# Kernel tuning notes

Measured on AMD Instinct MI355X. Metric: run time of the kernel, lower is better.

## Reference

```python
import jax, jax.numpy as jnp
import numpy as np
import math

H_MAX = 0.05  # hardcoded in ode_solve


def setup_inputs() -> dict:
    key = jax.random.key(0)
    k0, k1, k2, k3 = jax.random.split(key, 4)
    bs, dim, u_dim, hidden, time_len = 4096, 256, 64, 1024, 11
    z0 = jax.random.normal(k0, (bs, dim), jnp.float32)
    u = jax.random.normal(k1, (bs, u_dim), jnp.float32)
    t = jnp.arange(time_len, dtype=jnp.float32) * 0.05  # uniform grid, dt = h_max
    W1 = jax.random.normal(k2, (dim + u_dim, hidden), jnp.float32) / np.float32(np.sqrt(dim + u_dim))
    b1 = jnp.zeros((hidden,), jnp.float32)
    W2 = jax.random.normal(k3, (hidden, dim), jnp.float32) / np.float32(np.sqrt(hidden))
    b2 = jnp.zeros((dim,), jnp.float32)
    return {"z0": z0, "u": u, "t": t, "W1": W1, "b1": b1, "W2": W2, "b2": b2}


def reference(z0, u, t, W1, b1, W2, b2):
    """NeuralODE.forward with return_whole_sequence=True.
    Euler-integrates dz/dt = f(z, u, t) between consecutive grid points of t.
    f is the ODEF: tanh([z, u] @ W1 + b1) @ W2 + b2 (autonomous, stimulus-driven).
    Returns z of shape [time_len, bs, dim].
    """
    t_np = np.asarray(t)  # step counts are static (trace-time) quantities

    def f(z):  # [bs, dim] -> [bs, dim]
        h = jnp.tanh(jnp.concatenate([z, u], axis=-1) @ W1 + b1)
        return h @ W2 + b2

    zs = [z0]
    z = z0
    for i_t in range(t_np.shape[0] - 1):
        t0f, t1f = float(t_np[i_t]), float(t_np[i_t + 1])
        n_steps = int(math.ceil(abs(t1f - t0f) / H_MAX))
        h = jnp.float32((t1f - t0f) / n_steps)

        def euler_step(zc, _):
            return zc + h * f(zc), None

        z, _ = jax.lax.scan(euler_step, z, None, length=n_steps)
        zs.append(z)
    return jnp.stack(zs, axis=0)  # [time_len, bs, dim]
```

## Files before the change

kernel.cpp:

```cpp
#include <hip/hip_runtime.h>
#include <hip/hip_bf16.h>

#define BS   4096
#define DIM  256
#define UD   64
#define HID  1024
#define KCAT 320
#define ROWS 16

typedef __attribute__((ext_vector_type(8))) short bf16x8;
typedef __attribute__((ext_vector_type(4))) float f32x4;


__global__ void NeuralODE_91036126806381_kernel() {}

__device__ __forceinline__ float rd_any(const void* p, long idx, int isbf) {
    if (isbf) return __bfloat162float(((const __hip_bfloat16*)p)[idx]);
    return ((const float*)p)[idx];
}

__device__ __forceinline__ int sniff_bf16(const void* p) {
    const unsigned* w = (const unsigned*)p;
    int pass = 0;
    for (int i = 0; i < 64; ++i) {
        unsigned h = w[i] & 0xFFFFu;
        unsigned e = (h >> 7) & 0xFFu;
        if (h == 0u || h == 0x8000u || (e >= 96u && e <= 140u)) ++pass;
    }
    return pass >= 48 ? 1 : 0;
}

__device__ __forceinline__ float tanh_dev(float x) {
    float ax = fminf(fabsf(x), 15.0f);
    float e = __expf(-2.0f * ax);
    float r = (1.0f - e) * __builtin_amdgcn_rcpf(1.0f + e);
    return (x < 0.0f) ? -r : r;
}

__device__ __forceinline__ bf16x8 ld8(const __hip_bfloat16* p) {
    return *(const bf16x8*)p;
}

__global__ void plan_kernel(const void* __restrict__ t_raw,
                            const void* __restrict__ z0r,
                            const void* __restrict__ candA,
                            const void* __restrict__ candB,
                            const void* __restrict__ W1r,
                            float* __restrict__ h_arr, int* __restrict__ flags)
{
    if (threadIdx.x != 0 || blockIdx.x != 0) return;

    flags[0] = sniff_bf16(z0r);
    flags[1] = sniff_bf16(candA);
    flags[2] = sniff_bf16(candB);
    flags[3] = sniff_bf16(W1r);

    float mA = 0.0f;
    for (int i = 0; i < 256; ++i) {
        float v = fabsf(rd_any(candA, i, flags[1]));
        if (v > mA) mA = v;
    }
    flags[6] = (mA < 0.25f) ? 1 : 0;

    const unsigned tw0 = ((const unsigned*)t_raw)[0];
    const int t_bf16 = (tw0 != 0u) ? 1 : 0;

    float tv[11];
    for (int i = 0; i < 11; ++i) tv[i] = rd_any(t_raw, i, t_bf16);

    for (int i = 0; i < 10; ++i) {
        double dt = (double)tv[i + 1] - (double)tv[i];
        double r  = __builtin_fabs(dt) / 0.05;
        int n = (int)__builtin_ceil(r);
        if (n < 1) n = 1;
        if (n > 2) n = 2;
        float h = (float)(dt / (double)n);
        h_arr[2 * i]     = h;
        h_arr[2 * i + 1] = (n >= 2) ? h : 0.0f;
    }
}

__global__ __launch_bounds__(256) void prep_kernel(
    const void* __restrict__ W1r,
    const void* __restrict__ candA, const void* __restrict__ candB,
    const void* __restrict__ z0r,
    const void* __restrict__ b1r,  const void* __restrict__ b2r,
    const int* __restrict__ flags,
    __hip_bfloat16* __restrict__ w1p, __hip_bfloat16* __restrict__ w2p,
    __hip_bfloat16* __restrict__ zcat,
    float* __restrict__ zf, float* __restrict__ b1f, float* __restrict__ b2f,
    float* __restrict__ out0)
{
    const int swap = flags[6];
    const void* ur   = swap ? candB : candA;
    const void* W2r  = swap ? candA : candB;
    const int uflag  = swap ? flags[2] : flags[1];
    const int w2flag = swap ? flags[1] : flags[2];

    int i = blockIdx.x * 256 + threadIdx.x;
    if (i < 327680) {
        int k = i >> 10, n = i & 1023;
        int C = n >> 4, fm = n & 15;
        int kt = k >> 5, q = (k >> 3) & 3, e = k & 7;
        w1p[((C * 40 + kt * 4 + q) * 16 + fm) * 8 + e] =
            __float2bfloat16(rd_any(W1r, i, flags[3]));
    } else if (i < 589824) {
        int j = i - 327680;
        int k = j >> 8, n = j & 255;
        int C = n >> 4, fm = n & 15;
        int kt = k >> 5, q = (k >> 3) & 3, e = k & 7;
        w2p[((C * 128 + kt * 4 + q) * 16 + fm) * 8 + e] =
            __float2bfloat16(rd_any(W2r, j, w2flag));
    } else if (i < 851968) {
        int j = i - 589824;
        int r = j >> 6, c = j & 63;
        zcat[(long)r * KCAT + DIM + c] = __float2bfloat16(rd_any(ur, j, uflag));
    } else if (i < 1900544) {
        int j = i - 851968;
        int r = j >> 8, c = j & 255;
        float v = rd_any(z0r, j, flags[0]);
        zf[j] = v;
        zcat[(long)r * KCAT + c] = __float2bfloat16(v);
        out0[j] = v;
    } else if (i < 1901568) {
        int j = i - 1900544;
        b1f[j] = rd_any(b1r, j, sniff_bf16(b1r));
    } else if (i < 1901824) {
        int j = i - 1901568;
        b2f[j] = rd_any(b2r, j, sniff_bf16(b2r));
    }
}

__global__ __launch_bounds__(1024) void ode_kernel(
    const __hip_bfloat16* __restrict__ w1p,
    const __hip_bfloat16* __restrict__ w2p,
    const float* __restrict__ b1f, const float* __restrict__ b2f,
    const __hip_bfloat16* __restrict__ zcat0,
    const float* __restrict__ zf0,
    float* __restrict__ out,
    const float* __restrict__ h_arr)
{
    __shared__ __align__(16) __hip_bfloat16 apack[10 * 4 * 16 * 8];
    __shared__ __align__(16) __hip_bfloat16 Hpack[32 * 4 * 16 * 8];

    const int b0   = blockIdx.x * ROWS;
    const int tid  = threadIdx.x;
    const int lane = tid & 63;
    const int wv   = tid >> 6;
    const int fm   = lane & 15;
    const int q    = lane >> 4;
    const int cl   = lane & 15;
    const int rq   = (lane >> 4) * 4;

    for (int idx = tid; idx < ROWS * KCAT; idx += 1024) {
        int row = idx / KCAT, c = idx - row * KCAT;
        apack[(((c >> 5) * 4 + ((c & 31) >> 3)) * 16 + row) * 8 + (c & 7)] =
            zcat0[(long)(b0 + row) * KCAT + c];
    }

    float zreg[4];
#pragma unroll
    for (int r = 0; r < 4; ++r)
        zreg[r] = zf0[(long)(b0 + rq + r) * DIM + wv * 16 + cl];

    float b1r[4];
#pragma unroll
    for (int j = 0; j < 4; ++j) b1r[j] = b1f[(wv * 4 + j) * 16 + cl];
    const float b2r = b2f[wv * 16 + cl];

    __syncthreads();

    for (int iv = 0; iv < 10; ++iv) {
#pragma unroll 1
        for (int s = 0; s < 2; ++s) {
            const float h = h_arr[iv * 2 + s];
            if (h != 0.0f) {
                bf16x8 a[10];
#pragma unroll
                for (int kt = 0; kt < 10; ++kt)
                    a[kt] = *(const bf16x8*)&apack[((kt * 4 + q) * 16 + fm) * 8];

#pragma unroll
                for (int j = 0; j < 4; ++j) {
                    const int C = wv * 4 + j;
                    const __hip_bfloat16* wp =
                        w1p + ((long)(C * 40 + q) * 16 + fm) * 8;
                    f32x4 acc0 = (f32x4){0.f, 0.f, 0.f, 0.f};
                    f32x4 acc1 = (f32x4){0.f, 0.f, 0.f, 0.f};
#pragma unroll
                    for (int kt = 0; kt < 10; kt += 2) {
                        acc0 = __builtin_amdgcn_mfma_f32_16x16x32_bf16(
                            a[kt], ld8(wp + (long)kt * 512), acc0, 0, 0, 0);
                        acc1 = __builtin_amdgcn_mfma_f32_16x16x32_bf16(
                            a[kt + 1], ld8(wp + (long)(kt + 1) * 512), acc1, 0, 0, 0);
                    }
                    const int colb = C * 16 + cl;
                    const int hbase =
                        ((colb >> 5) * 4 + ((colb & 31) >> 3)) * 128 + (colb & 7);
#pragma unroll
                    for (int r = 0; r < 4; ++r) {
                        float v = acc0[r] + acc1[r] + b1r[j];
                        Hpack[hbase + (rq + r) * 8] = __float2bfloat16(tanh_dev(v));
                    }
                }
                __syncthreads();

                f32x4 zacc0 = (f32x4){0.f, 0.f, 0.f, 0.f};
                f32x4 zacc1 = (f32x4){0.f, 0.f, 0.f, 0.f};
                const __hip_bfloat16* wq =
                    w2p + ((long)(wv * 128 + q) * 16 + fm) * 8;
#pragma unroll 8
                for (int kt = 0; kt < 32; kt += 2) {
                    bf16x8 aH0 = *(const bf16x8*)&Hpack[((kt * 4 + q) * 16 + fm) * 8];
                    bf16x8 aH1 = *(const bf16x8*)&Hpack[(((kt + 1) * 4 + q) * 16 + fm) * 8];
                    zacc0 = __builtin_amdgcn_mfma_f32_16x16x32_bf16(
                        aH0, ld8(wq + (long)kt * 512), zacc0, 0, 0, 0);
                    zacc1 = __builtin_amdgcn_mfma_f32_16x16x32_bf16(
                        aH1, ld8(wq + (long)(kt + 1) * 512), zacc1, 0, 0, 0);
                }

                const int col = wv * 16 + cl;
                const int abase =
                    ((col >> 5) * 4 + ((col & 31) >> 3)) * 128 + (col & 7);
#pragma unroll
                for (int r = 0; r < 4; ++r) {
                    float v = zreg[r] + h * (zacc0[r] + zacc1[r] + b2r);
                    zreg[r] = v;
                    apack[abase + (rq + r) * 8] = __float2bfloat16(v);
                }
                __syncthreads();
            }
        }
        float* os = out + (long)(iv + 1) * BS * DIM;
#pragma unroll
        for (int r = 0; r < 4; ++r)
            os[(long)(b0 + rq + r) * DIM + wv * 16 + cl] = zreg[r];
    }
}

extern "C" void kernel_launch(void* const* d_in, const int* in_sizes, int n_in,
                              void* d_out, int out_size, void* d_ws, size_t ws_size,
                              hipStream_t stream) {
    const void *z0 = 0, *t = 0, *W1 = 0, *b1 = 0, *b2 = 0;
    const void *candA = 0, *candB = 0;
    for (int i = 0; i < n_in; ++i) {
        int s = in_sizes[i];
        if      (s == 1048576) z0 = d_in[i];
        else if (s == 327680)  W1 = d_in[i];
        else if (s == 262144)  { if (!candA) candA = d_in[i]; else candB = d_in[i]; }
        else if (s == 1024)    b1 = d_in[i];
        else if (s == 256)     b2 = d_in[i];
        else if (s == 11)      t  = d_in[i];
    }
    if (!z0 || !W1 || !candA || !candB || !b1 || !b2 || !t) {
        z0 = d_in[0]; candA = d_in[1]; t = d_in[2];
        W1 = d_in[3]; b1 = d_in[4]; candB = d_in[5]; b2 = d_in[6];
    }

    float* out = (float*)d_out;

    char* ws = (char*)d_ws;
    int*            flags = (int*)  (ws + 0);
    float*          h_arr = (float*)(ws + 64);
    float*          b1f   = (float*)(ws + 4096);
    float*          b2f   = (float*)(ws + 8192);
    __hip_bfloat16* w1p   = (__hip_bfloat16*)(ws + 16384);
    __hip_bfloat16* w2p   = (__hip_bfloat16*)(ws + 671744);
    __hip_bfloat16* zcat  = (__hip_bfloat16*)(ws + 1196032);
    float*          zf    = (float*)         (ws + 3817472);

    plan_kernel<<<1, 64, 0, stream>>>(t, z0, candA, candB, W1, h_arr, flags);
    prep_kernel<<<7429, 256, 0, stream>>>(W1, candA, candB, z0, b1, b2, flags,
                                          w1p, w2p, zcat, zf, b1f, b2f, out);

    ode_kernel<<<256, 1024, 0, stream>>>(w1p, w2p, b1f, b2f, zcat, zf,
                                         out, h_arr);
}
```

Baseline: 295.8 us.

## Stream weight tiles through per-wave LDS ring with async global-to-LDS loads

Replaces direct global loads of W1/W2 fragments feeding MFMA with a per-wave 4-slot LDS ring filled by global_load_lds, issuing loads three tiles ahead under manual vmcnt/lgkmcnt waits. The W1 phase prefetches the first W2 tiles so the second GEMM starts with data in flight. It also caches the step sizes in shared memory and replaces __syncthreads with explicit waitcnt plus s_barrier. The aim is to hide weight-load latency behind MFMA work. The cost is 64KB of extra LDS and fragile hand-written wait counts that depend on instruction ordering.

Measured after the change: 538.4 us. 1.82x slower.

```diff
diff --git a/kernel.cpp b/kernel.cpp
--- a/kernel.cpp
+++ b/kernel.cpp
@@ -37,9 +37,25 @@
     return (x < 0.0f) ? -r : r;
 }
 
-__device__ __forceinline__ bf16x8 ld8(const __hip_bfloat16* p) {
-    return *(const bf16x8*)p;
-}
+__device__ __forceinline__ void gload_lds16(const __hip_bfloat16* g,
+                                            __hip_bfloat16* l) {
+    __builtin_amdgcn_global_load_lds(
+        (const __attribute__((address_space(1))) void*)g,
+        (__attribute__((address_space(3))) void*)l, 16, 0, 0);
+}
+
+__device__ __forceinline__ void waitvm(int n) {
+    if (n <= 0)      asm volatile("s_waitcnt vmcnt(0)" ::: "memory");
+    else if (n == 1) asm volatile("s_waitcnt vmcnt(1)" ::: "memory");
+    else             asm volatile("s_waitcnt vmcnt(2)" ::: "memory");
+}
+__device__ __forceinline__ void waitlgkm(int n) {
+    if (n <= 0)      asm volatile("s_waitcnt lgkmcnt(0)" ::: "memory");
+    else if (n == 1) asm volatile("s_waitcnt lgkmcnt(1)" ::: "memory");
+    else             asm volatile("s_waitcnt lgkmcnt(2)" ::: "memory");
+}
+
+#define MFMA __builtin_amdgcn_mfma_f32_16x16x32_bf16
 
 __global__ void plan_kernel(const void* __restrict__ t_raw,
                             const void* __restrict__ z0r,
@@ -140,15 +156,15 @@
     float* __restrict__ out,
     const float* __restrict__ h_arr)
 {
-    __shared__ __align__(16) __hip_bfloat16 apack[10 * 4 * 16 * 8];
-    __shared__ __align__(16) __hip_bfloat16 Hpack[32 * 4 * 16 * 8];
+    __shared__ __align__(16) __hip_bfloat16 apack[10 * 512];
+    __shared__ __align__(16) __hip_bfloat16 Hpack[32 * 512];
+    __shared__ __align__(16) __hip_bfloat16 ring[16 * 4 * 512];
+    __shared__ float hsm[20];
 
     const int b0   = blockIdx.x * ROWS;
     const int tid  = threadIdx.x;
     const int lane = tid & 63;
     const int wv   = tid >> 6;
-    const int fm   = lane & 15;
-    const int q    = lane >> 4;
     const int cl   = lane & 15;
     const int rq   = (lane >> 4) * 4;
 
@@ -157,6 +173,7 @@
         apack[(((c >> 5) * 4 + ((c & 31) >> 3)) * 16 + row) * 8 + (c & 7)] =
             zcat0[(long)(b0 + row) * KCAT + c];
     }
+    if (tid < 20) hsm[tid] = h_arr[tid];
 
     float zreg[4];
 #pragma unroll
@@ -168,33 +185,50 @@
     for (int j = 0; j < 4; ++j) b1r[j] = b1f[(wv * 4 + j) * 16 + cl];
     const float b2r = b2f[wv * 16 + cl];
 
+    const __hip_bfloat16* gA = w1p + (long)wv * 20480 + lane * 8;
+    const __hip_bfloat16* gB = w2p + (long)wv * 16384 + lane * 8;
+    __hip_bfloat16* ringw = &ring[wv * 2048];
+
     __syncthreads();
 
+#pragma unroll 1
     for (int iv = 0; iv < 10; ++iv) {
 #pragma unroll 1
         for (int s = 0; s < 2; ++s) {
-            const float h = h_arr[iv * 2 + s];
+            const float h = hsm[iv * 2 + s];
             if (h != 0.0f) {
+                gload_lds16(gA + 0 * 512, ringw + 0 * 512);
+                gload_lds16(gA + 1 * 512, ringw + 1 * 512);
+                gload_lds16(gA + 2 * 512, ringw + 2 * 512);
+
                 bf16x8 a[10];
 #pragma unroll
                 for (int kt = 0; kt < 10; ++kt)
-                    a[kt] = *(const bf16x8*)&apack[((kt * 4 + q) * 16 + fm) * 8];
+                    a[kt] = *(const bf16x8*)&apack[kt * 512 + lane * 8];
 
 #pragma unroll
                 for (int j = 0; j < 4; ++j) {
-                    const int C = wv * 4 + j;
-                    const __hip_bfloat16* wp =
-                        w1p + ((long)(C * 40 + q) * 16 + fm) * 8;
                     f32x4 acc0 = (f32x4){0.f, 0.f, 0.f, 0.f};
                     f32x4 acc1 = (f32x4){0.f, 0.f, 0.f, 0.f};
 #pragma unroll
-                    for (int kt = 0; kt < 10; kt += 2) {
-                        acc0 = __builtin_amdgcn_mfma_f32_16x16x32_bf16(
-                            a[kt], ld8(wp + (long)kt * 512), acc0, 0, 0, 0);
-                        acc1 = __builtin_amdgcn_mfma_f32_16x16x32_bf16(
-                            a[kt + 1], ld8(wp + (long)(kt + 1) * 512), acc1, 0, 0, 0);
+                    for (int kt = 0; kt < 10; ++kt) {
+                        const int c = j * 10 + kt;
+                        waitvm(2);
+                        bf16x8 bv = *(const bf16x8*)
+                            &ringw[(c & 3) * 512 + lane * 8];
+                        waitlgkm(1);
+                        if (c + 3 < 40) {
+                            const int c2 = c + 3;
+                            gload_lds16(gA + (c2 / 10) * 5120 + (c2 % 10) * 512,
+                                        ringw + (c2 & 3) * 512);
+                        } else {
+                            const int d = c - 37;
+                            gload_lds16(gB + d * 512, ringw + (d & 3) * 512);
+                        }
+                        if (kt & 1) acc1 = MFMA(a[kt], bv, acc1, 0, 0, 0);
+                        else        acc0 = MFMA(a[kt], bv, acc0, 0, 0, 0);
                     }
-                    const int colb = C * 16 + cl;
+                    const int colb = (wv * 4 + j) * 16 + cl;
                     const int hbase =
                         ((colb >> 5) * 4 + ((colb & 31) >> 3)) * 128 + (colb & 7);
 #pragma unroll
@@ -203,20 +237,23 @@
                         Hpack[hbase + (rq + r) * 8] = __float2bfloat16(tanh_dev(v));
                     }
                 }
-                __syncthreads();
+                asm volatile("s_waitcnt lgkmcnt(0)" ::: "memory");
+                __builtin_amdgcn_s_barrier();
 
                 f32x4 zacc0 = (f32x4){0.f, 0.f, 0.f, 0.f};
                 f32x4 zacc1 = (f32x4){0.f, 0.f, 0.f, 0.f};
-                const __hip_bfloat16* wq =
-                    w2p + ((long)(wv * 128 + q) * 16 + fm) * 8;
-#pragma unroll 8
-                for (int kt = 0; kt < 32; kt += 2) {
-                    bf16x8 aH0 = *(const bf16x8*)&Hpack[((kt * 4 + q) * 16 + fm) * 8];
-                    bf16x8 aH1 = *(const bf16x8*)&Hpack[(((kt + 1) * 4 + q) * 16 + fm) * 8];
-                    zacc0 = __builtin_amdgcn_mfma_f32_16x16x32_bf16(
-                        aH0, ld8(wq + (long)kt * 512), zacc0, 0, 0, 0);
-                    zacc1 = __builtin_amdgcn_mfma_f32_16x16x32_bf16(
-                        aH1, ld8(wq + (long)(kt + 1) * 512), zacc1, 0, 0, 0);
+#pragma unroll
+                for (int kt = 0; kt < 32; ++kt) {
+                    waitvm(kt <= 29 ? 2 : 31 - kt);
+                    bf16x8 bv = *(const bf16x8*)
+                        &ringw[(kt & 3) * 512 + lane * 8];
+                    bf16x8 aH = *(const bf16x8*)&Hpack[kt * 512 + lane * 8];
+                    waitlgkm(2);
+                    if (kt + 3 < 32)
+                        gload_lds16(gB + (kt + 3) * 512,
+                                    ringw + ((kt + 3) & 3) * 512);
+                    if (kt & 1) zacc1 = MFMA(aH, bv, zacc1, 0, 0, 0);
+                    else        zacc0 = MFMA(aH, bv, zacc0, 0, 0, 0);
                 }
 
                 const int col = wv * 16 + cl;
@@ -228,7 +265,8 @@
                     zreg[r] = v;
                     apack[abase + (rq + r) * 8] = __float2bfloat16(v);
                 }
-                __syncthreads();
+                asm volatile("s_waitcnt lgkmcnt(0)" ::: "memory");
+                __builtin_amdgcn_s_barrier();
             }
         }
         float* os = out + (long)(iv + 1) * BS * DIM;
```
